# Kernel optimization log

Hardware: AMD Instinct MI355X
Metric: run time of the kernel (lower is better)

Reference implementation:

```python
import jax, jax.numpy as jnp
import numpy as np


def setup_inputs() -> dict:
    key = jax.random.key(0)
    ks = jax.random.split(key, 5)
    B, S, D, O = 8, 2048, 1024, 1024
    q = jax.random.normal(ks[0], (B, S, D), dtype=jnp.float32)
    k = jax.random.normal(ks[1], (B, S, D), dtype=jnp.float32)
    # glorot-scale weights
    scale = (2.0 / (D + O)) ** 0.5
    Wq = jax.random.normal(ks[2], (D, O), dtype=jnp.float32) * scale
    Wk = jax.random.normal(ks[3], (D, O), dtype=jnp.float32) * scale
    Wv = jax.random.normal(ks[4], (D, O), dtype=jnp.float32) * scale
    return {"q": q, "k": k, "Wq": Wq, "Wk": Wk, "Wv": Wv}


def reference(q, k, Wq, Wk, Wv):
    # q: [B, S, Dq], k: [B, S, Dk]
    q_proj = jnp.einsum('bsd,do->bso', q, Wq)   # [B, S, O]
    k_proj = jnp.einsum('bsd,do->bso', k, Wk)   # [B, S, O]
    v_proj = jnp.einsum('bsd,do->bso', k, Wv)   # [B, S, O]
    # Dot(axes=-1): contract feature dims -> [B, Sq, Sk]; NO 1/sqrt(d) scaling
    attn = jnp.einsum('bqo,bko->bqk', q_proj, k_proj)
    attn_w = jax.nn.softmax(attn, axis=-1)      # softmax over key axis
    # Dot(axes=1): contracts the QUERY axis of attn with the seq axis of v (attn^T @ v)
    context = jnp.einsum('bqk,bqo->bko', attn_w, v_proj)  # [B, S, O]
    return jnp.concatenate([q, context], axis=-1)  # [B, S, Dq + O]
```

## Files before the change

kernel.cpp:

```cpp
#include <hip/hip_runtime.h>
#include <hip/hip_bf16.h>


typedef __attribute__((ext_vector_type(4))) float f32x4;
typedef __attribute__((ext_vector_type(16))) float f32x16;
typedef _Float16 f16;
typedef __attribute__((ext_vector_type(8))) _Float16 f16x8;
typedef __attribute__((ext_vector_type(4))) _Float16 f16x4;

#define LOG2E 1.4426950408889634f

#define CM_F32     0
#define CM_F16     1
#define CM_F16T    3
#define CM_ATTN    4
#define CM_PROJ3   5
#define CM_PVS     6

#define STAGE(WHICH, KS, KT, BO) do { \
    const char* _gb = (WHICH) ? Bb : Ab; \
    const int _ld = (WHICH) ? ldb : lda; \
    const long _r = (WHICH) ? (long)(bn + srow0) : (long)(bm + srow0); \
    const int _k0 = (KT) * 64 + (KS) * 32 + sh8; \
    char* _dst = (char*)smem + (BO) + (WHICH) * 32768 + (KS) * 16384 + wave * 1024; \
    const char* _g0 = _gb + ((_r * _ld + _k0) << 1); \
    const char* _g1 = _gb + (((_r + 128) * _ld + _k0) << 1); \
    __builtin_amdgcn_global_load_lds((const __attribute__((address_space(1))) void*)_g0, \
        (__attribute__((address_space(3))) void*)_dst, 16, 0, 0); \
    __builtin_amdgcn_global_load_lds((const __attribute__((address_space(1))) void*)_g1, \
        (__attribute__((address_space(3))) void*)(_dst + 8192), 16, 0, 0); \
} while (0)

#define GPHASE2(KS, STAGE_CODE, VM) do { \
    f16x8 af[2][4], bb[2][2], sv[2]; \
    _Pragma("unroll") \
    for (int s = 0; s < 2; ++s) { \
        _Pragma("unroll") \
        for (int mt = 0; mt < 4; ++mt) \
            af[s][mt] = *(const f16x8*)(smem + \
                ((bufo + (KS) * 16384 + abase[mt]) ^ (s << 5))); \
        _Pragma("unroll") \
        for (int nt = 0; nt < 2; ++nt) \
            bb[s][nt] = *(const f16x8*)(smem + \
                ((bufo + (KS) * 16384 + bbase[nt]) ^ (s << 5))); \
        if (CMODE == CM_PVS) \
            sv[s] = *(const f16x8*)(smem + 131072 + wm * 4096 + \
                t * 128 + (KS) * 64 + s * 32 + (h5 << 4)); \
    } \
    STAGE_CODE; \
    __builtin_amdgcn_s_barrier(); \
    if (CMODE == CM_PVS) { \
        _Pragma("unroll") \
        for (int s = 0; s < 2; ++s) \
            _Pragma("unroll") \
            for (int mt = 0; mt < 4; ++mt) \
                af[s][mt] *= sv[s]; \
    } \
    __builtin_amdgcn_s_setprio(1); \
    _Pragma("unroll") \
    for (int s = 0; s < 2; ++s) \
        _Pragma("unroll") \
        for (int mt = 0; mt < 4; ++mt) \
            _Pragma("unroll") \
            for (int nt = 0; nt < 2; ++nt) \
                acc[mt][nt] = __builtin_amdgcn_mfma_f32_32x32x16_f16( \
                    af[s][mt], bb[s][nt], acc[mt][nt], 0, 0, 0); \
    __builtin_amdgcn_s_setprio(0); \
    VM; \
    __builtin_amdgcn_s_barrier(); \
} while (0)

template<int CMODE>
__global__ __launch_bounds__(512, 2)
void gemm256(const f16* __restrict__ A, const f16* __restrict__ B,
             void* __restrict__ Cv,
             int M, int N, int K, int lda, int ldb, int ldc,
             long az, long bz, long cz,
             float* __restrict__ pm, float* __restrict__ ps)
{
    __shared__ __align__(16) char smem[139264];

    const int z = blockIdx.z;
    const char* Ab;
    const char* Bb;
    if (CMODE == CM_PROJ3) {
        const int y = blockIdx.y;
        Ab = (const char*)(A + (y ? (long)M * 1024 : 0));
        Bb = (const char*)(B + (long)y * 1024 * 1024);
    } else {
        Ab = (const char*)(A + z * az);
        Bb = (const char*)(B + z * bz);
    }

    const int nbx = N >> 8;
    int wg = blockIdx.x;
    const int nwg = gridDim.x;
    if ((nwg & 7) == 0) wg = (wg & 7) * (nwg >> 3) + (wg >> 3);
    const int bm = (wg / nbx) << 8;
    const int bn = (wg % nbx) << 8;

    const int tid = threadIdx.x;
    const int wave = tid >> 6;
    const int lane = tid & 63;
    const int l31 = lane & 31;
    const int h5 = lane >> 5;
    const int wm = wave >> 2;
    const int wn = wave & 3;

    const int f3 = (l31 ^ (l31 >> 2)) & 3;
    const int sl = ((h5 ^ f3) << 4);
    int abase[4], bbase[2];
    #pragma unroll
    for (int mt = 0; mt < 4; ++mt)
        abase[mt] = (wm * 128 + mt * 32 + l31) * 64 + sl;
    #pragma unroll
    for (int nt = 0; nt < 2; ++nt)
        bbase[nt] = 32768 + (wn * 64 + nt * 32 + l31) * 64 + sl;

    const int srow0 = tid >> 2;
    const int sh8 = ((tid ^ (tid >> 2) ^ (tid >> 4)) & 3) * 8;

    f32x16 acc[4][2];
    #pragma unroll
    for (int mt = 0; mt < 4; ++mt)
        #pragma unroll
        for (int nt = 0; nt < 2; ++nt)
            acc[mt][nt] = (f32x16)(0.f);

    const int nt_k = K >> 6;

    {
        if (CMODE == CM_PVS) {
            const char* gsc = (const char*)ps +
                (((long)z * 16 + (bm >> 7)) * 2048) * 2 + tid * 16;
            __builtin_amdgcn_global_load_lds(
                (const __attribute__((address_space(1))) void*)gsc,
                (__attribute__((address_space(3))) void*)
                    ((char*)smem + 131072 + wave * 1024), 16, 0, 0);
        }
        const int t1p = (nt_k > 1) ? 1 : 0;
        STAGE(0, 0, 0, 0);
        STAGE(1, 0, 0, 0);
        STAGE(0, 1, 0, 0);
        STAGE(1, 1, 0, 0);
        STAGE(0, 0, t1p, 65536);
        STAGE(1, 0, t1p, 65536);
        asm volatile("s_waitcnt vmcnt(4)" ::: "memory");
        __builtin_amdgcn_s_barrier();
    }

    for (int t = 0; t < nt_k; ++t) {
        const int bufo = (t & 1) << 16;
        const int nbo = bufo ^ 65536;
        const int t1 = (t + 1 < nt_k) ? t + 1 : nt_k - 1;
        const int t2 = (t + 2 < nt_k) ? t + 2 : nt_k - 1;
        GPHASE2(0, { STAGE(0, 1, t1, nbo); STAGE(1, 1, t1, nbo); }, );
        GPHASE2(1, { STAGE(0, 0, t2, bufo); STAGE(1, 0, t2, bufo); },
                asm volatile("s_waitcnt vmcnt(4)" ::: "memory"));
    }
    asm volatile("s_waitcnt vmcnt(0)" ::: "memory");

    if (CMODE == CM_ATTN) {
        f16* E = (f16*)Cv + z * cz;
        #pragma unroll
        for (int nt = 0; nt < 2; ++nt) {
            float Mx = -3.4e38f;
            #pragma unroll
            for (int mt = 0; mt < 4; ++mt)
                #pragma unroll
                for (int r = 0; r < 16; ++r)
                    Mx = fmaxf(Mx, acc[mt][nt][r]);
            Mx = fmaxf(Mx, __shfl_xor(Mx, 32, 64));
            float Sm = 0.f;
            #pragma unroll
            for (int mt = 0; mt < 4; ++mt)
                #pragma unroll
                for (int r = 0; r < 16; ++r) {
                    const float e = exp2f((acc[mt][nt][r] - Mx) * LOG2E);
                    acc[mt][nt][r] = e;
                    Sm += e;
                }
            Sm += __shfl_xor(Sm, 32, 64);
            const int col = bn + wn * 64 + nt * 32 + l31;
            #pragma unroll
            for (int mt = 0; mt < 4; ++mt) {
                const int row0 = bm + wm * 128 + mt * 32 + h5 * 4;
                #pragma unroll
                for (int rq = 0; rq < 4; ++rq)
                    #pragma unroll
                    for (int rr = 0; rr < 4; ++rr)
                        E[(long)(row0 + rq * 8 + rr) * ldc + col] =
                            (f16)acc[mt][nt][rq * 4 + rr];
            }
            if (lane < 32) {
                const long pidx = ((long)z * 16 + (bm >> 7) + wm) * N + col;
                pm[pidx] = Mx * LOG2E;
                ps[pidx] = Sm;
            }
        }
        return;
    }

    #pragma unroll
    for (int mt = 0; mt < 4; ++mt) {
        #pragma unroll
        for (int nt = 0; nt < 2; ++nt) {
            const int row0 = bm + wm * 128 + mt * 32 + h5 * 4;
            const int col = bn + wn * 64 + nt * 32 + l31;
            if (CMODE == CM_F32 || CMODE == CM_PVS) {
                float* C = (float*)Cv + z * cz;
                #pragma unroll
                for (int rq = 0; rq < 4; ++rq)
                    #pragma unroll
                    for (int rr = 0; rr < 4; ++rr)
                        C[(long)(row0 + rq * 8 + rr) * ldc + col] =
                            acc[mt][nt][rq * 4 + rr];
            } else if (CMODE == CM_F16) {
                f16* C = (f16*)Cv + z * cz;
                #pragma unroll
                for (int rq = 0; rq < 4; ++rq)
                    #pragma unroll
                    for (int rr = 0; rr < 4; ++rr)
                        C[(long)(row0 + rq * 8 + rr) * ldc + col] =
                            (f16)acc[mt][nt][rq * 4 + rr];
            } else if (CMODE == CM_F16T) {
                f16* C = (f16*)Cv + z * cz;
                #pragma unroll
                for (int rq = 0; rq < 4; ++rq) {
                    f16x4 v;
                    #pragma unroll
                    for (int rr = 0; rr < 4; ++rr) v[rr] = (f16)acc[mt][nt][rq * 4 + rr];
                    *(f16x4*)(C + (long)col * ldc + row0 + rq * 8) = v;
                }
            } else {
                const int y = blockIdx.y;
                if (y < 2) {
                    f16* C = (f16*)Cv + (long)y * M * 1024;
                    #pragma unroll
                    for (int rq = 0; rq < 4; ++rq)
                        #pragma unroll
                        for (int rr = 0; rr < 4; ++rr)
                            C[(long)(row0 + rq * 8 + rr) * 1024 + col] =
                                (f16)acc[mt][nt][rq * 4 + rr];
                } else {
                    f16* C = (f16*)pm;
                    #pragma unroll
                    for (int rq = 0; rq < 4; ++rq) {
                        f16x4 v;
                        #pragma unroll
                        for (int rr = 0; rr < 4; ++rr)
                            v[rr] = (f16)acc[mt][nt][rq * 4 + rr];
                        *(f16x4*)(C + (long)col * M + row0 + rq * 8) = v;
                    }
                }
            }
        }
    }
}

__global__ __launch_bounds__(256)
void pack_cast_qk(const float* __restrict__ qin, const float* __restrict__ kin,
                  f16* __restrict__ qp, f16* __restrict__ kp,
                  float* __restrict__ oq, long nquads)
{
    const long i = (long)blockIdx.x * 256 + threadIdx.x;
    if (i >= 2 * nquads) return;
    const int isK = (i >= nquads);
    const long j = isK ? i - nquads : i;
    const long row = j >> 8;
    const int c = (int)(j & 255) * 4;
    const float4 v = isK ? *(const float4*)(kin + row * 1024 + c)
                         : *(const float4*)(qin + row * 1024 + c);
    f16x4 h;
    h[0] = (f16)v.x; h[1] = (f16)v.y; h[2] = (f16)v.z; h[3] = (f16)v.w;
    if (isK) {
        *(f16x4*)(kp + row * 1024 + c) = h;
    } else {
        *(float4*)(oq + row * 2048 + c) = v;
        *(f16x4*)(qp + row * 1024 + c) = h;
    }
}

__global__ __launch_bounds__(256)
void pack_W_T(const float* __restrict__ W, f16* __restrict__ Wt)
{
    __shared__ float tile[64][65];
    const int d0 = blockIdx.y * 64, o0 = blockIdx.x * 64;
    const int t = threadIdx.x;
    const int rr = t >> 4, c4 = (t & 15) * 4;
    #pragma unroll
    for (int it = 0; it < 4; ++it) {
        const int r = rr + it * 16;
        const float4 v = *(const float4*)(W + (long)(d0 + r) * 1024 + o0 + c4);
        tile[r][c4] = v.x; tile[r][c4 + 1] = v.y;
        tile[r][c4 + 2] = v.z; tile[r][c4 + 3] = v.w;
    }
    __syncthreads();
    #pragma unroll
    for (int it = 0; it < 4; ++it) {
        const int orow = rr + it * 16;
        f16x4 h;
        #pragma unroll
        for (int j = 0; j < 4; ++j) h[j] = (f16)tile[c4 + j][orow];
        *(f16x4*)(Wt + (long)(o0 + orow) * 1024 + d0 + c4) = h;
    }
}

__global__ __launch_bounds__(256)
void softmax_merge16(const float* __restrict__ pm, const float* __restrict__ ps,
                     f16* __restrict__ scale, int nq)
{
    const int idx = blockIdx.x * 256 + threadIdx.x;
    if (idx >= nq) return;
    const int z = idx >> 11, q = idx & 2047;
    const float* pmz = pm + ((long)z * 16) * 2048 + q;
    const float* psz = ps + ((long)z * 16) * 2048 + q;
    float mx = -3.4e38f;
    #pragma unroll
    for (int j = 0; j < 16; ++j) mx = fmaxf(mx, pmz[j * 2048]);
    float s = 0.f;
    #pragma unroll
    for (int j = 0; j < 16; ++j)
        s += psz[j * 2048] * exp2f(pmz[j * 2048] - mx);
    const float L = mx + log2f(s);
    f16* sc = scale + ((long)z * 16) * 2048 + q;
    #pragma unroll
    for (int j = 0; j < 16; ++j)
        sc[j * 2048] = (f16)exp2f(pmz[j * 2048] - L);
}

__global__ __launch_bounds__(256)
void copy_q_kernel(const float* __restrict__ q, float* __restrict__ out, long n4)
{
    const long idx = (long)blockIdx.x * 256 + threadIdx.x;
    if (idx >= n4) return;
    const long row = idx >> 8;
    const long c4 = idx & 255;
    *(float4*)(&out[row * 2048 + c4 * 4]) =
        *(const float4*)(&q[row * 1024 + c4 * 4]);
}

#define BM 64
#define BN 64
#define BKF 16
template<int opA, int opB>
__global__ __launch_bounds__(256)
void sgemm(const float* __restrict__ A, const float* __restrict__ B,
           float* __restrict__ C,
           int M, int N, int K, int lda, int ldb, int ldc)
{
    __shared__ float As[BKF][BM];
    __shared__ float Bs[BKF][BN];
    const int tid = threadIdx.x;
    const int tx = tid & 15, ty = tid >> 4;
    const int bm = blockIdx.y * BM, bn = blockIdx.x * BN;
    float acc[4][4] = {};
    for (int k0 = 0; k0 < K; k0 += BKF) {
        if (opA == 0) {
            const int row = tid >> 2, kq = (tid & 3) * 4;
            const float4 v = *(const float4*)(A + (long)(bm + row) * lda + (k0 + kq));
            As[kq + 0][row] = v.x; As[kq + 1][row] = v.y;
            As[kq + 2][row] = v.z; As[kq + 3][row] = v.w;
        } else {
            const int kk = tid >> 4, mq = (tid & 15) * 4;
            *(float4*)(&As[kk][mq]) =
                *(const float4*)(A + (long)(k0 + kk) * lda + (bm + mq));
        }
        if (opB == 0) {
            const int kk = tid >> 4, nq = (tid & 15) * 4;
            *(float4*)(&Bs[kk][nq]) =
                *(const float4*)(B + (long)(k0 + kk) * ldb + (bn + nq));
        } else {
            const int row = tid >> 2, kq = (tid & 3) * 4;
            const float4 v = *(const float4*)(B + (long)(bn + row) * ldb + (k0 + kq));
            Bs[kq + 0][row] = v.x; Bs[kq + 1][row] = v.y;
            Bs[kq + 2][row] = v.z; Bs[kq + 3][row] = v.w;
        }
        __syncthreads();
        #pragma unroll
        for (int kk = 0; kk < BKF; ++kk) {
            const float4 a = *(const float4*)(&As[kk][ty * 4]);
            const float4 b = *(const float4*)(&Bs[kk][tx * 4]);
            const float av[4] = {a.x, a.y, a.z, a.w};
            const float bv[4] = {b.x, b.y, b.z, b.w};
            #pragma unroll
            for (int i = 0; i < 4; ++i)
                #pragma unroll
                for (int j = 0; j < 4; ++j)
                    acc[i][j] += av[i] * bv[j];
        }
        __syncthreads();
    }
    #pragma unroll
    for (int i = 0; i < 4; ++i) {
        const float4 v = make_float4(acc[i][0], acc[i][1], acc[i][2], acc[i][3]);
        *(float4*)(&C[(long)(bm + ty * 4 + i) * ldc + (bn + tx * 4)]) = v;
    }
}

__device__ __forceinline__ float wave_reduce_max(float v) {
    #pragma unroll
    for (int off = 1; off < 64; off <<= 1)
        v = fmaxf(v, __shfl_xor(v, off, 64));
    return v;
}
__device__ __forceinline__ float wave_reduce_sum(float v) {
    #pragma unroll
    for (int off = 1; off < 64; off <<= 1)
        v += __shfl_xor(v, off, 64);
    return v;
}

__global__ __launch_bounds__(256)
void softmax_rows2048(float* __restrict__ X)
{
    float* x = X + (long)blockIdx.x * 2048;
    const int tid = threadIdx.x;
    float4 v0 = *(const float4*)(&x[tid * 4]);
    float4 v1 = *(const float4*)(&x[1024 + tid * 4]);
    float m = fmaxf(fmaxf(fmaxf(v0.x, v0.y), fmaxf(v0.z, v0.w)),
                    fmaxf(fmaxf(v1.x, v1.y), fmaxf(v1.z, v1.w)));
    m = wave_reduce_max(m);
    __shared__ float sm[4];
    __shared__ float ss[4];
    const int wid = tid >> 6;
    if ((tid & 63) == 0) sm[wid] = m;
    __syncthreads();
    m = fmaxf(fmaxf(sm[0], sm[1]), fmaxf(sm[2], sm[3]));
    v0.x = expf(v0.x - m); v0.y = expf(v0.y - m);
    v0.z = expf(v0.z - m); v0.w = expf(v0.w - m);
    v1.x = expf(v1.x - m); v1.y = expf(v1.y - m);
    v1.z = expf(v1.z - m); v1.w = expf(v1.w - m);
    float s = (v0.x + v0.y + v0.z + v0.w) + (v1.x + v1.y + v1.z + v1.w);
    s = wave_reduce_sum(s);
    if ((tid & 63) == 0) ss[wid] = s;
    __syncthreads();
    s = ss[0] + ss[1] + ss[2] + ss[3];
    const float inv = 1.0f / s;
    v0.x *= inv; v0.y *= inv; v0.z *= inv; v0.w *= inv;
    v1.x *= inv; v1.y *= inv; v1.z *= inv; v1.w *= inv;
    *(float4*)(&x[tid * 4]) = v0;
    *(float4*)(&x[1024 + tid * 4]) = v1;
}

static void fallback_fp32(const float* q, const float* k, const float* Wq,
                          const float* Wk, const float* Wv, float* out,
                          void* d_ws, hipStream_t stream)
{
    const int S = 2048, D = 1024, O = 1024, B = 8;
    float* qp = (float*)d_ws;
    float* kp = qp + (size_t)S * O;
    float* vp = kp + (size_t)S * O;
    float* attn = vp + (size_t)S * O;
    const long n4 = (long)B * S * D / 4;
    copy_q_kernel<<<dim3((n4 + 255) / 256), 256, 0, stream>>>(q, out, n4);
    const dim3 blk(256);
    const dim3 gproj(O / BN, S / BM), gattn(S / BN, S / BM), gctx(O / BN, S / BM);
    for (int b = 0; b < B; ++b) {
        const float* qb = q + (size_t)b * S * D;
        const float* kb = k + (size_t)b * S * D;
        float* outc = out + (size_t)b * S * 2048 + D;
        sgemm<0, 0><<<gproj, blk, 0, stream>>>(qb, Wq, qp, S, O, D, D, O, O);
        sgemm<0, 0><<<gproj, blk, 0, stream>>>(kb, Wk, kp, S, O, D, D, O, O);
        sgemm<0, 0><<<gproj, blk, 0, stream>>>(kb, Wv, vp, S, O, D, D, O, O);
        sgemm<0, 1><<<gattn, blk, 0, stream>>>(qp, kp, attn, S, S, O, O, O, S);
        softmax_rows2048<<<dim3(S), blk, 0, stream>>>(attn);
        sgemm<1, 0><<<gctx, blk, 0, stream>>>(attn, vp, outc, S, O, S, S, O, 2048);
    }
}

extern "C" void kernel_launch(void* const* d_in, const int* in_sizes, int n_in,
                              void* d_out, int out_size, void* d_ws, size_t ws_size,
                              hipStream_t stream)
{
    const float* q  = (const float*)d_in[0];
    const float* k  = (const float*)d_in[1];
    const float* Wq = (const float*)d_in[2];
    const float* Wk = (const float*)d_in[3];
    const float* Wv = (const float*)d_in[4];
    float* out = (float*)d_out;

    const int B = 8, S = 2048;

    auto need = [](int g) -> size_t {
        const size_t wpk = 3 * (size_t)1024 * 1024 * 2;
        const size_t pkA = (size_t)g * 2048 * 1024 * 2;
        const size_t vpT = (size_t)1024 * g * 2048 * 2;
        const size_t aw  = (size_t)g * 2048 * 2048 * 2;
        const size_t pp  = 2 * (size_t)g * 16 * 2048 * 4 + (size_t)g * 16 * 2048 * 2;
        return wpk + 4 * pkA + vpT + aw + pp + 32 * 256;
    };
    int g = 0;
    for (int cand : {8, 4, 2, 1})
        if (need(cand) <= ws_size) { g = cand; break; }
    if (g == 0) { fallback_fp32(q, k, Wq, Wk, Wv, out, d_ws, stream); return; }

    char* p = (char*)d_ws;
    auto carve = [&](size_t bytes) {
        char* r = p;
        p += (bytes + 255) & ~(size_t)255;
        return r;
    };
    f16* Wtq = (f16*)carve((size_t)1024 * 1024 * 2);
    f16* Wtk = (f16*)carve((size_t)1024 * 1024 * 2);
    f16* Wtv = (f16*)carve((size_t)1024 * 1024 * 2);
    const size_t pkAB = (size_t)g * 2048 * 1024 * 2;
    f16* qpack   = (f16*)carve(pkAB);
    f16* kpack   = (f16*)carve(pkAB);
    f16* qp_pack = (f16*)carve(pkAB);
    f16* kp_pack = (f16*)carve(pkAB);
    f16* vpT     = (f16*)carve((size_t)1024 * g * 2048 * 2);
    f16* attn_w  = (f16*)carve((size_t)g * 2048 * 2048 * 2);
    float* pmb   = (float*)carve((size_t)g * 16 * 2048 * 4);
    float* psb   = (float*)carve((size_t)g * 16 * 2048 * 4);
    f16* scb     = (f16*)carve((size_t)g * 16 * 2048 * 2);

    pack_W_T<<<dim3(16, 16), 256, 0, stream>>>(Wq, Wtq);
    pack_W_T<<<dim3(16, 16), 256, 0, stream>>>(Wk, Wtk);
    pack_W_T<<<dim3(16, 16), 256, 0, stream>>>(Wv, Wtv);

    const int Mg = g * 2048;
    const dim3 blk(256);
    const dim3 blk512(512);
    const long zSS = (long)2048 * 2048;
    const long zSD = (long)2048 * 1024;

    for (int gi = 0; gi < B / g; ++gi) {
        const float* qg = q + (size_t)gi * Mg * 1024;
        const float* kg = k + (size_t)gi * Mg * 1024;
        float* outq = out + (size_t)gi * Mg * 2048;

        const long nquads = (long)Mg * 256;
        pack_cast_qk<<<dim3((2 * nquads + 255) / 256), blk, 0, stream>>>(
            qg, kg, qpack, kpack, outq, nquads);

        const dim3 g1((1024 / 256) * (Mg / 256), 3, 1);
        gemm256<CM_PROJ3><<<g1, blk512, 0, stream>>>(
            qpack, Wtq, qp_pack, Mg, 1024, 1024, 1024, 1024, 1024, 0, 0, 0,
            (float*)vpT, nullptr);

        const dim3 g2((2048 / 256) * (2048 / 256), 1, g);
        gemm256<CM_ATTN><<<g2, blk512, 0, stream>>>(
            kp_pack, qp_pack, attn_w, 2048, 2048, 1024, 1024, 1024, 2048,
            zSD, zSD, zSS, pmb, psb);

        const int nq = g * 2048;
        softmax_merge16<<<dim3((nq + 255) / 256), blk, 0, stream>>>(pmb, psb, scb, nq);

        float* outg = out + (size_t)gi * Mg * 2048 + 1024;
        const dim3 g3((1024 / 256) * (2048 / 256), 1, g);
        gemm256<CM_PVS><<<g3, blk512, 0, stream>>>(
            attn_w, vpT, outg, 2048, 1024, 2048, 2048, Mg, 2048,
            zSS, 2048, zSS, nullptr, (float*)scb);
    }
}
```

Before: 362.1 us.

## Fold Wq·Wk^T into a precomputed matrix to drop the K projection GEMM

Precomputes G = Wq·Wk^T once with a split-K GEMM plus a reduction kernel. Each batch then projects q by G and feeds raw k directly into the attention GEMM, so the projection GEMM shrinks from three outputs to two. This removes about a third of the projection FLOPs per batch, at the cost of extra setup kernels and different fp16 rounding through G. The GEMM inner phase is also reordered so the async LDS staging is issued after the barrier, overlapping with the MFMA block.

```diff
diff --git a/kernel.cpp b/kernel.cpp
--- a/kernel.cpp
+++ b/kernel.cpp
@@ -14,7 +14,7 @@
 #define CM_F16     1
 #define CM_F16T    3
 #define CM_ATTN    4
-#define CM_PROJ3   5
+#define CM_PROJ2   5
 #define CM_PVS     6
 
 #define STAGE(WHICH, KS, KT, BO) do { \
@@ -47,8 +47,6 @@
             sv[s] = *(const f16x8*)(smem + 131072 + wm * 4096 + \
                 t * 128 + (KS) * 64 + s * 32 + (h5 << 4)); \
     } \
-    STAGE_CODE; \
-    __builtin_amdgcn_s_barrier(); \
     if (CMODE == CM_PVS) { \
         _Pragma("unroll") \
         for (int s = 0; s < 2; ++s) \
@@ -56,7 +54,9 @@
             for (int mt = 0; mt < 4; ++mt) \
                 af[s][mt] *= sv[s]; \
     } \
+    __builtin_amdgcn_s_barrier(); \
     __builtin_amdgcn_s_setprio(1); \
+    STAGE_CODE; \
     _Pragma("unroll") \
     for (int s = 0; s < 2; ++s) \
         _Pragma("unroll") \
@@ -83,7 +83,7 @@
     const int z = blockIdx.z;
     const char* Ab;
     const char* Bb;
-    if (CMODE == CM_PROJ3) {
+    if (CMODE == CM_PROJ2) {
         const int y = blockIdx.y;
         Ab = (const char*)(A + (y ? (long)M * 1024 : 0));
         Bb = (const char*)(B + (long)y * 1024 * 1024);
@@ -234,8 +234,8 @@
                 }
             } else {
                 const int y = blockIdx.y;
-                if (y < 2) {
-                    f16* C = (f16*)Cv + (long)y * M * 1024;
+                if (y == 0) {
+                    f16* C = (f16*)Cv;
                     #pragma unroll
                     for (int rq = 0; rq < 4; ++rq)
                         #pragma unroll
@@ -282,6 +282,19 @@
 }
 
 __global__ __launch_bounds__(256)
+void cast_f16(const float* __restrict__ in, f16* __restrict__ outp, long nquads)
+{
+    const long i = (long)blockIdx.x * 256 + threadIdx.x;
+    if (i >= nquads) return;
+    const long row = i >> 8;
+    const int c = (int)(i & 255) * 4;
+    const float4 v = *(const float4*)(in + row * 1024 + c);
+    f16x4 h;
+    h[0] = (f16)v.x; h[1] = (f16)v.y; h[2] = (f16)v.z; h[3] = (f16)v.w;
+    *(f16x4*)(outp + row * 1024 + c) = h;
+}
+
+__global__ __launch_bounds__(256)
 void pack_W_T(const float* __restrict__ W, f16* __restrict__ Wt)
 {
     __shared__ float tile[64][65];
@@ -304,6 +317,22 @@
         for (int j = 0; j < 4; ++j) h[j] = (f16)tile[c4 + j][orow];
         *(f16x4*)(Wt + (long)(o0 + orow) * 1024 + d0 + c4) = h;
     }
+}
+
+__global__ __launch_bounds__(256)
+void gt_reduce(const float* __restrict__ P, f16* __restrict__ Gt, long nquads)
+{
+    const long i = (long)blockIdx.x * 256 + threadIdx.x;
+    if (i >= nquads) return;
+    float4 s = *(const float4*)(P + i * 4);
+    #pragma unroll
+    for (int z = 1; z < 8; ++z) {
+        const float4 v = *(const float4*)(P + (long)z * 1048576 + i * 4);
+        s.x += v.x; s.y += v.y; s.z += v.z; s.w += v.w;
+    }
+    f16x4 h;
+    h[0] = (f16)s.x; h[1] = (f16)s.y; h[2] = (f16)s.z; h[3] = (f16)s.w;
+    *(f16x4*)(Gt + i * 4) = h;
 }
 
 __global__ __launch_bounds__(256)
@@ -483,12 +512,13 @@
     const int B = 8, S = 2048;
 
     auto need = [](int g) -> size_t {
-        const size_t wpk = 3 * (size_t)1024 * 1024 * 2;
+        const size_t fixed = ((size_t)1024 * 1024 * 2) * 4
+                           + (size_t)8 * 1024 * 1024 * 4;
         const size_t pkA = (size_t)g * 2048 * 1024 * 2;
         const size_t vpT = (size_t)1024 * g * 2048 * 2;
         const size_t aw  = (size_t)g * 2048 * 2048 * 2;
         const size_t pp  = 2 * (size_t)g * 16 * 2048 * 4 + (size_t)g * 16 * 2048 * 2;
-        return wpk + 4 * pkA + vpT + aw + pp + 32 * 256;
+        return fixed + 3 * pkA + vpT + aw + pp + 32 * 256;
     };
     int g = 0;
     for (int cand : {8, 4, 2, 1})
@@ -501,27 +531,33 @@
         p += (bytes + 255) & ~(size_t)255;
         return r;
     };
-    f16* Wtq = (f16*)carve((size_t)1024 * 1024 * 2);
-    f16* Wtk = (f16*)carve((size_t)1024 * 1024 * 2);
-    f16* Wtv = (f16*)carve((size_t)1024 * 1024 * 2);
+    f16* Gt   = (f16*)carve((size_t)1024 * 1024 * 2);
+    f16* Wtv  = (f16*)carve((size_t)1024 * 1024 * 2);
+    f16* Wq_h = (f16*)carve((size_t)1024 * 1024 * 2);
+    f16* Wk_h = (f16*)carve((size_t)1024 * 1024 * 2);
+    float* Gp = (float*)carve((size_t)8 * 1024 * 1024 * 4);
     const size_t pkAB = (size_t)g * 2048 * 1024 * 2;
-    f16* qpack   = (f16*)carve(pkAB);
-    f16* kpack   = (f16*)carve(pkAB);
-    f16* qp_pack = (f16*)carve(pkAB);
-    f16* kp_pack = (f16*)carve(pkAB);
-    f16* vpT     = (f16*)carve((size_t)1024 * g * 2048 * 2);
-    f16* attn_w  = (f16*)carve((size_t)g * 2048 * 2048 * 2);
-    float* pmb   = (float*)carve((size_t)g * 16 * 2048 * 4);
-    float* psb   = (float*)carve((size_t)g * 16 * 2048 * 4);
-    f16* scb     = (f16*)carve((size_t)g * 16 * 2048 * 2);
-
-    pack_W_T<<<dim3(16, 16), 256, 0, stream>>>(Wq, Wtq);
-    pack_W_T<<<dim3(16, 16), 256, 0, stream>>>(Wk, Wtk);
-    pack_W_T<<<dim3(16, 16), 256, 0, stream>>>(Wv, Wtv);
-
-    const int Mg = g * 2048;
+    f16* qpack  = (f16*)carve(pkAB);
+    f16* kpack  = (f16*)carve(pkAB);
+    f16* qG     = (f16*)carve(pkAB);
+    f16* vpT    = (f16*)carve((size_t)1024 * g * 2048 * 2);
+    f16* attn_w = (f16*)carve((size_t)g * 2048 * 2048 * 2);
+    float* pmb  = (float*)carve((size_t)g * 16 * 2048 * 4);
+    float* psb  = (float*)carve((size_t)g * 16 * 2048 * 4);
+    f16* scb    = (f16*)carve((size_t)g * 16 * 2048 * 2);
+
     const dim3 blk(256);
     const dim3 blk512(512);
+
+    pack_W_T<<<dim3(16, 16), blk, 0, stream>>>(Wv, Wtv);
+    cast_f16<<<dim3(1024), blk, 0, stream>>>(Wq, Wq_h, 1024 * 256);
+    cast_f16<<<dim3(1024), blk, 0, stream>>>(Wk, Wk_h, 1024 * 256);
+    gemm256<CM_F32><<<dim3(16, 1, 8), blk512, 0, stream>>>(
+        Wk_h, Wq_h, Gp, 1024, 1024, 128, 1024, 1024, 1024,
+        128, 128, (long)1024 * 1024, nullptr, nullptr);
+    gt_reduce<<<dim3(1024), blk, 0, stream>>>(Gp, Gt, 1024 * 256);
+
+    const int Mg = g * 2048;
     const long zSS = (long)2048 * 2048;
     const long zSD = (long)2048 * 1024;
 
@@ -534,14 +570,14 @@
         pack_cast_qk<<<dim3((2 * nquads + 255) / 256), blk, 0, stream>>>(
             qg, kg, qpack, kpack, outq, nquads);
 
-        const dim3 g1((1024 / 256) * (Mg / 256), 3, 1);
-        gemm256<CM_PROJ3><<<g1, blk512, 0, stream>>>(
-            qpack, Wtq, qp_pack, Mg, 1024, 1024, 1024, 1024, 1024, 0, 0, 0,
+        const dim3 g1((1024 / 256) * (Mg / 256), 2, 1);
+        gemm256<CM_PROJ2><<<g1, blk512, 0, stream>>>(
+            qpack, Gt, qG, Mg, 1024, 1024, 1024, 1024, 1024, 0, 0, 0,
             (float*)vpT, nullptr);
 
         const dim3 g2((2048 / 256) * (2048 / 256), 1, g);
         gemm256<CM_ATTN><<<g2, blk512, 0, stream>>>(
-            kp_pack, qp_pack, attn_w, 2048, 2048, 1024, 1024, 1024, 2048,
+            kpack, qG, attn_w, 2048, 2048, 1024, 1024, 1024, 2048,
             zSD, zSD, zSS, pmb, psb);
 
         const int nq = g * 2048;
```

Result: faster. 348.1 us (median of 2 runs) (-3.9%).
